# Kernel tuning notes

Measured on AMD Instinct MI355X. Metric: run time of the kernel, lower is better.

The kernel has to match this reference:

```python
import jax, jax.numpy as jnp
import numpy as np

WIN = 7
NP_ = WIN * WIN
COV_NORM = NP_ / (NP_ - 1)

def _box(x, w):
    # valid 7x7 box filter, NCHW, single channel
    return jax.lax.conv_general_dilated(
        x, w, window_strides=(1, 1), padding='VALID',
        dimension_numbers=('NCHW', 'OIHW', 'NCHW'))

def setup_inputs() -> dict:
    key = jax.random.key(0)
    k1, k2, k3, k4 = jax.random.split(key, 4)
    N, H, W = 64, 384, 384
    X = jax.random.uniform(k1, (N, 1, H, W), dtype=jnp.float32)
    Y = jax.random.uniform(k2, (N, 1, H, W), dtype=jnp.float32)
    norm = jax.random.uniform(k3, (N,), dtype=jnp.float32)
    mx = jax.random.uniform(k4, (N,), dtype=jnp.float32) + 0.5
    w = jnp.ones((1, 1, WIN, WIN), dtype=jnp.float32) / NP_
    return {"X": X, "Y": Y, "norm": norm, "max": mx, "w": w}

def reference(X, Y, norm, max, w):
    q = 100000.0
    X = X * q
    Y = Y * q
    mx = max * q
    data_range = mx[:, None, None, None]
    C1 = (0.01 * data_range) ** 2
    C2 = (0.03 * data_range) ** 2
    ux = _box(X, w)
    uy = _box(Y, w)
    uxx = _box(X * X, w)
    uyy = _box(Y * Y, w)
    uxy = _box(X * Y, w)
    vx = COV_NORM * (uxx - ux * ux)
    vy = COV_NORM * (uyy - uy * uy)
    vxy = COV_NORM * (uxy - ux * uy)
    A1 = 2 * ux * uy + C1
    A2 = 2 * vxy + C2
    B1 = ux ** 2 + uy ** 2 + C1
    B2 = vx + vy + C2
    S = (A1 * A2) / (B1 * B2)
    return -jnp.mean(S)
```

## Files before the change

kernel.cpp:

```cpp
#include <hip/hip_runtime.h>


constexpr int IND   = 384;
constexpr int OUTD  = 378;
constexpr int RB    = 14;
constexpr int BANDS = OUTD / RB;
constexpr int CPL   = 6;

using f32x2 = __attribute__((ext_vector_type(2))) float;

__global__ __launch_bounds__(64, 2)
void ssim_band(const float* __restrict__ X, const float* __restrict__ Y,
               const float* __restrict__ MX, float* __restrict__ blocksum)
{
    const int band = blockIdx.x;
    const int n    = blockIdx.y;
    const int lane = threadIdx.x;
    const int c0   = lane * CPL;
    const int r0   = band * RB;

    const float* __restrict__ Xp = X + (size_t)n * (IND * IND) + c0;
    const float* __restrict__ Yp = Y + (size_t)n * (IND * IND) + c0;

    float hx[7][CPL], hy[7][CPL];
    float sx[CPL]  = {}, sy[CPL]  = {};
    float sxx[CPL] = {}, syy[CPL] = {}, sxy[CPL] = {};

#define LOADROW(DX, DY, R) {                                                  \
    const float* _px = Xp + (size_t)(R) * IND;                                \
    const float* _py = Yp + (size_t)(R) * IND;                                \
    f32x2 _a = *(const f32x2*)_px;                                            \
    f32x2 _b = *(const f32x2*)(_px + 2);                                      \
    f32x2 _c = *(const f32x2*)(_px + 4);                                      \
    f32x2 _d = *(const f32x2*)_py;                                            \
    f32x2 _e = *(const f32x2*)(_py + 2);                                      \
    f32x2 _f = *(const f32x2*)(_py + 4);                                      \
    DX[0]=_a.x; DX[1]=_a.y; DX[2]=_b.x; DX[3]=_b.y; DX[4]=_c.x; DX[5]=_c.y;   \
    DY[0]=_d.x; DY[1]=_d.y; DY[2]=_e.x; DY[3]=_e.y; DY[4]=_f.x; DY[5]=_f.y; }

#pragma unroll
    for (int k = 0; k < 7; ++k) LOADROW(hx[k], hy[k], r0 + k)

    float pax[CPL], pay[CPL], pbx[CPL], pby[CPL];
    LOADROW(pax, pay, r0 + 7)
    LOADROW(pbx, pby, r0 + 8)

#pragma unroll
    for (int k = 0; k < 7; ++k)
#pragma unroll
        for (int c = 0; c < CPL; ++c) {
            float x = hx[k][c], y = hy[k][c];
            sx[c] += x;  sy[c] += y;
            sxx[c] = fmaf(x, x, sxx[c]);
            syy[c] = fmaf(y, y, syy[c]);
            sxy[c] = fmaf(x, y, sxy[c]);
        }

    const float m   = MX[n];
    const float c1  = (0.01f * m) * (0.01f * m);
    const float c2  = (0.03f * m) * (0.03f * m);
    const float k1  = 2401.0f * c1;
    const float k2  = 2401.0f * c2;
    const float cn  = 49.0f / 48.0f;
    const float cn2 = 2.0f * cn;

#define HSUM(S, O) {                                                          \
    float _n0 = __shfl_down(S[0], 1), _n1 = __shfl_down(S[1], 1);             \
    float _n2 = __shfl_down(S[2], 1), _n3 = __shfl_down(S[3], 1);             \
    float _n4 = __shfl_down(S[4], 1), _n5 = __shfl_down(S[5], 1);             \
    float _t  = ((S[0]+S[1]) + (S[2]+S[3])) + (S[4]+S[5]);                    \
    O[0] = _t   + _n0;                                                        \
    O[1] = O[0] - S[0] + _n1;                                                 \
    O[2] = O[1] - S[1] + _n2;                                                 \
    O[3] = O[2] - S[2] + _n3;                                                 \
    O[4] = O[3] - S[3] + _n4;                                                 \
    O[5] = O[4] - S[4] + _n5; }

    float partial = 0.f;

    for (int kk = 0; kk < RB / 7; ++kk) {
#pragma unroll
        for (int i = 0; i < 7; ++i) {
            float t1[CPL], t2[CPL], t3[CPL], t4[CPL], t5[CPL];
            HSUM(sx,  t1) HSUM(sy,  t2) HSUM(sxx, t3) HSUM(syy, t4) HSUM(sxy, t5)

            if (lane < 63) {
#pragma unroll
                for (int c = 0; c < CPL; ++c) {
                    float pxy = t1[c] * t2[c];
                    float ss  = fmaf(t1[c], t1[c], t2[c] * t2[c]);
                    float A1  = fmaf(2.f, pxy, k1);
                    float B1  = ss + k1;
                    float A2  = fmaf(cn2, fmaf(49.f, t5[c], -pxy), k2);
                    float B2  = fmaf(cn, fmaf(49.f, t3[c] + t4[c], -ss), k2);
                    partial += __fdividef(A1 * A2, B1 * B2);
                }
            }

#pragma unroll
            for (int c = 0; c < CPL; ++c) {
                float nx = pax[c], ny = pay[c];
                float ox = hx[i][c], oy = hy[i][c];
                sx[c] += nx - ox;
                sy[c] += ny - oy;
                sxx[c] = fmaf(nx, nx, fmaf(-ox, ox, sxx[c]));
                syy[c] = fmaf(ny, ny, fmaf(-oy, oy, syy[c]));
                sxy[c] = fmaf(nx, ny, fmaf(-ox, oy, sxy[c]));
                hx[i][c] = nx;  hy[i][c] = ny;
                pax[c] = pbx[c]; pay[c] = pby[c];
            }
            int nr = r0 + 7 * kk + i + 9;
            if (nr > IND - 1) nr = IND - 1;
            LOADROW(pbx, pby, nr)
        }
    }
#undef HSUM
#undef LOADROW

#pragma unroll
    for (int off = 32; off; off >>= 1) partial += __shfl_down(partial, off);
    if (lane == 0) blocksum[(size_t)n * BANDS + band] = partial;
}

__global__ __launch_bounds__(256)
void ssim_reduce(const float* __restrict__ blocksum, float* __restrict__ out,
                 int nblocks, float inv_npix)
{
    const int tid = threadIdx.x;
    float s = 0.f;
    for (int i = tid; i < nblocks; i += 256) s += blocksum[i];
#pragma unroll
    for (int off = 32; off; off >>= 1) s += __shfl_down(s, off);
    __shared__ float ws[4];
    if ((tid & 63) == 0) ws[tid >> 6] = s;
    __syncthreads();
    if (tid == 0) out[0] = -(ws[0] + ws[1] + ws[2] + ws[3]) * inv_npix;
}

extern "C" void kernel_launch(void* const* d_in, const int* in_sizes, int n_in,
                              void* d_out, int out_size, void* d_ws, size_t ws_size,
                              hipStream_t stream)
{
    const float* X  = (const float*)d_in[0];
    const float* Y  = (const float*)d_in[1];
    const float* MX = (const float*)d_in[3];

    const int N       = in_sizes[3];
    const int nblocks = N * BANDS;

    float* bs = (float*)d_ws;

    dim3 grid(BANDS, N);
    ssim_band<<<grid, 64, 0, stream>>>(X, Y, MX, bs);

    const float inv_npix = 1.0f / ((float)N * OUTD * OUTD);
    ssim_reduce<<<1, 256, 0, stream>>>(bs, (float*)d_out, nblocks, inv_npix);
}
```

Before: 30.18 us.

## Drop 7-row register history, reload outgoing rows, halve band height

Removes the 7-row register ring buffer of X/Y values and instead re-reads the row leaving the sliding window from global memory (cache), cutting register use. Band height drops from 14 to 7 rows and launch bounds ask for 4 blocks per CU, giving twice as many blocks and higher occupancy. The cost is extra global/L2 loads per output row and more halo rows re-read per band, since each band re-primes 6 rows for only 7 outputs.

```diff
diff --git a/kernel.cpp b/kernel.cpp
--- a/kernel.cpp
+++ b/kernel.cpp
@@ -3,13 +3,13 @@
 
 constexpr int IND   = 384;
 constexpr int OUTD  = 378;
-constexpr int RB    = 14;
+constexpr int RB    = 7;
 constexpr int BANDS = OUTD / RB;
 constexpr int CPL   = 6;
 
 using f32x2 = __attribute__((ext_vector_type(2))) float;
 
-__global__ __launch_bounds__(64, 2)
+__global__ __launch_bounds__(64, 4)
 void ssim_band(const float* __restrict__ X, const float* __restrict__ Y,
                const float* __restrict__ MX, float* __restrict__ blocksum)
 {
@@ -21,10 +21,6 @@
 
     const float* __restrict__ Xp = X + (size_t)n * (IND * IND) + c0;
     const float* __restrict__ Yp = Y + (size_t)n * (IND * IND) + c0;
-
-    float hx[7][CPL], hy[7][CPL];
-    float sx[CPL]  = {}, sy[CPL]  = {};
-    float sxx[CPL] = {}, syy[CPL] = {}, sxy[CPL] = {};
 
 #define LOADROW(DX, DY, R) {                                                  \
     const float* _px = Xp + (size_t)(R) * IND;                                \
@@ -38,23 +34,29 @@
     DX[0]=_a.x; DX[1]=_a.y; DX[2]=_b.x; DX[3]=_b.y; DX[4]=_c.x; DX[5]=_c.y;   \
     DY[0]=_d.x; DY[1]=_d.y; DY[2]=_e.x; DY[3]=_e.y; DY[4]=_f.x; DY[5]=_f.y; }
 
+    float rx[6][CPL], ry[6][CPL];
 #pragma unroll
-    for (int k = 0; k < 7; ++k) LOADROW(hx[k], hy[k], r0 + k)
+    for (int k = 0; k < 6; ++k) LOADROW(rx[k], ry[k], r0 + k)
 
     float pax[CPL], pay[CPL], pbx[CPL], pby[CPL];
-    LOADROW(pax, pay, r0 + 7)
-    LOADROW(pbx, pby, r0 + 8)
+    float oax[CPL], oay[CPL];
+    LOADROW(pax, pay, r0 + 6)
+    LOADROW(pbx, pby, r0 + 7)
 
+    float sx[CPL]  = {}, sy[CPL]  = {};
+    float sxx[CPL] = {}, syy[CPL] = {}, sxy[CPL] = {};
 #pragma unroll
-    for (int k = 0; k < 7; ++k)
+    for (int k = 0; k < 6; ++k)
 #pragma unroll
         for (int c = 0; c < CPL; ++c) {
-            float x = hx[k][c], y = hy[k][c];
+            float x = rx[k][c], y = ry[k][c];
             sx[c] += x;  sy[c] += y;
             sxx[c] = fmaf(x, x, sxx[c]);
             syy[c] = fmaf(y, y, syy[c]);
             sxy[c] = fmaf(x, y, sxy[c]);
         }
+#pragma unroll
+    for (int c = 0; c < CPL; ++c) { oax[c] = rx[0][c]; oay[c] = ry[0][c]; }
 
     const float m   = MX[n];
     const float c1  = (0.01f * m) * (0.01f * m);
@@ -78,40 +80,47 @@
 
     float partial = 0.f;
 
-    for (int kk = 0; kk < RB / 7; ++kk) {
 #pragma unroll
-        for (int i = 0; i < 7; ++i) {
-            float t1[CPL], t2[CPL], t3[CPL], t4[CPL], t5[CPL];
-            HSUM(sx,  t1) HSUM(sy,  t2) HSUM(sxx, t3) HSUM(syy, t4) HSUM(sxy, t5)
+    for (int i = 0; i < RB; ++i) {
+#pragma unroll
+        for (int c = 0; c < CPL; ++c) {
+            float nx = pax[c], ny = pay[c];
+            sx[c] += nx;  sy[c] += ny;
+            sxx[c] = fmaf(nx, nx, sxx[c]);
+            syy[c] = fmaf(ny, ny, syy[c]);
+            sxy[c] = fmaf(nx, ny, sxy[c]);
+        }
 
-            if (lane < 63) {
-#pragma unroll
-                for (int c = 0; c < CPL; ++c) {
-                    float pxy = t1[c] * t2[c];
-                    float ss  = fmaf(t1[c], t1[c], t2[c] * t2[c]);
-                    float A1  = fmaf(2.f, pxy, k1);
-                    float B1  = ss + k1;
-                    float A2  = fmaf(cn2, fmaf(49.f, t5[c], -pxy), k2);
-                    float B2  = fmaf(cn, fmaf(49.f, t3[c] + t4[c], -ss), k2);
-                    partial += __fdividef(A1 * A2, B1 * B2);
-                }
-            }
+        float t1[CPL], t2[CPL], t3[CPL], t4[CPL], t5[CPL];
+        HSUM(sx,  t1) HSUM(sy,  t2) HSUM(sxx, t3) HSUM(syy, t4) HSUM(sxy, t5)
 
 #pragma unroll
+        for (int c = 0; c < CPL; ++c) {
+            float ox = oax[c], oy = oay[c];
+            sx[c] -= ox;  sy[c] -= oy;
+            sxx[c] = fmaf(-ox, ox, sxx[c]);
+            syy[c] = fmaf(-oy, oy, syy[c]);
+            sxy[c] = fmaf(-ox, oy, sxy[c]);
+            pax[c] = pbx[c];  pay[c] = pby[c];
+        }
+        {
+            int nr = r0 + 8 + i;  if (nr > IND - 1) nr = IND - 1;
+            LOADROW(pbx, pby, nr)
+            int orr = r0 + 1 + i;
+            LOADROW(oax, oay, orr)
+        }
+
+        if (lane < 63) {
+#pragma unroll
             for (int c = 0; c < CPL; ++c) {
-                float nx = pax[c], ny = pay[c];
-                float ox = hx[i][c], oy = hy[i][c];
-                sx[c] += nx - ox;
-                sy[c] += ny - oy;
-                sxx[c] = fmaf(nx, nx, fmaf(-ox, ox, sxx[c]));
-                syy[c] = fmaf(ny, ny, fmaf(-oy, oy, syy[c]));
-                sxy[c] = fmaf(nx, ny, fmaf(-ox, oy, sxy[c]));
-                hx[i][c] = nx;  hy[i][c] = ny;
-                pax[c] = pbx[c]; pay[c] = pby[c];
+                float pxy = t1[c] * t2[c];
+                float ss  = fmaf(t1[c], t1[c], t2[c] * t2[c]);
+                float A1  = fmaf(2.f, pxy, k1);
+                float B1  = ss + k1;
+                float A2  = fmaf(cn2, fmaf(49.f, t5[c], -pxy), k2);
+                float B2  = fmaf(cn, fmaf(49.f, t3[c] + t4[c], -ss), k2);
+                partial += __fdividef(A1 * A2, B1 * B2);
             }
-            int nr = r0 + 7 * kk + i + 9;
-            if (nr > IND - 1) nr = IND - 1;
-            LOADROW(pbx, pby, nr)
         }
     }
 #undef HSUM
```

After: 46.29 us. 53.4% more time.
